# Optimization experiments

Measured on AMD Instinct MI355X. Metric: run time of the kernel, lower is better.

The kernel has to match this reference:

```python
import jax, jax.numpy as jnp
import numpy as np

B, N, D, H = 4, 512, 4, 256


def _linear_params(key, fan_in, fan_out):
    # torch.nn.Linear default init: U(-1/sqrt(fan_in), 1/sqrt(fan_in))
    lim = 1.0 / np.sqrt(fan_in)
    kw, kb = jax.random.split(key)
    W = jax.random.uniform(kw, (fan_in, fan_out), minval=-lim, maxval=lim, dtype=jnp.float32)
    b = jax.random.uniform(kb, (fan_out,), minval=-lim, maxval=lim, dtype=jnp.float32)
    return W, b


def setup_inputs() -> dict:
    key = jax.random.key(0)
    ks = jax.random.split(key, 8)
    x = jax.random.normal(ks[0], (B, N, D), dtype=jnp.float32)
    adj = jax.random.uniform(ks[1], (B, N, N), dtype=jnp.float32)  # soft adjacency in [0,1)
    W_e1, b_e1 = _linear_params(ks[2], 2 * D, H)
    W_e2, b_e2 = _linear_params(ks[3], H, H)
    W_n1, b_n1 = _linear_params(ks[4], H, H)
    W_n2, b_n2 = _linear_params(ks[5], H, H)
    W_o1, b_o1 = _linear_params(ks[6], D + H, H)
    W_o, b_o = _linear_params(ks[7], H, D)
    return {
        "x": x, "adj": adj,
        "W_e1": W_e1, "b_e1": b_e1, "W_e2": W_e2, "b_e2": b_e2,
        "W_n1": W_n1, "b_n1": b_n1, "W_n2": W_n2, "b_n2": b_n2,
        "W_o1": W_o1, "b_o1": b_o1, "W_o": W_o, "b_o": b_o,
    }


def reference(x, adj, W_e1, b_e1, W_e2, b_e2, W_n1, b_n1, W_n2, b_n2, W_o1, b_o1, W_o, b_o):
    b_, n_, d_ = x.shape
    # innode[b,i,j,:] = x[b,j]; outnode[b,i,j,:] = x[b,i]
    innode = jnp.broadcast_to(x[:, None, :, :], (b_, n_, n_, d_))
    outnode = jnp.broadcast_to(x[:, :, None, :], (b_, n_, n_, d_))
    edge_in = jnp.concatenate([innode, outnode], axis=-1)          # [B,N,N,2D]
    node2edge = jax.nn.relu(edge_in @ W_e1 + b_e1)                 # [B,N,N,H]
    edge2edge = jax.nn.relu(node2edge @ W_e2 + b_e2)               # [B,N,N,H]
    # adjacency-masked sum over axis 1 (the i axis)
    agg = jnp.einsum('bij,bijh->bjh', adj, edge2edge)              # [B,N,H]
    out1 = jax.nn.relu(agg @ W_n1 + b_n1)
    out2 = jax.nn.relu(out1 @ W_n2 + b_n2)
    out3 = jnp.concatenate([x, out2], axis=-1)                     # [B,N,D+H]
    out4 = out3 @ W_o1 + b_o1
    out5 = out4 @ W_o + b_o                                        # [B,N,D]
    # CONTINUOUS is False for the classifier variant
    return jax.nn.log_softmax(out5, axis=2)
```

## Files before the change

### kernel.cpp

```cpp
#include <hip/hip_runtime.h>
#include <hip/hip_fp16.h>
#include <math.h>

#define Bq 4
#define Nq 512
#define Dq 4
#define Hq 256

typedef _Float16 f16x8 __attribute__((ext_vector_type(8)));
typedef float f32x4 __attribute__((ext_vector_type(4)));

__device__ __forceinline__ f16x8 hadd_relu(f16x8 u, f16x8 v) {
    f16x8 s = u + v;
    const f16x8 z = (f16x8)(_Float16)0.0f;
    return __builtin_elementwise_max(s, z);
}

__global__ __launch_bounds__(256) void prep_uv(
    const float* __restrict__ x, const float* __restrict__ We1,
    const float* __restrict__ be1, __half* __restrict__ U, __half* __restrict__ V) {
    const int bn = blockIdx.x;
    const int k = threadIdx.x;
    const float* xp = x + bn * Dq;
    const float x0 = xp[0], x1 = xp[1], x2 = xp[2], x3 = xp[3];
    float u = be1[k];
    u = fmaf(x0, We1[0 * 256 + k], u);
    u = fmaf(x1, We1[1 * 256 + k], u);
    u = fmaf(x2, We1[2 * 256 + k], u);
    u = fmaf(x3, We1[3 * 256 + k], u);
    float v = x0 * We1[4 * 256 + k];
    v = fmaf(x1, We1[5 * 256 + k], v);
    v = fmaf(x2, We1[6 * 256 + k], v);
    v = fmaf(x3, We1[7 * 256 + k], v);
    U[(size_t)bn * Hq + k] = __float2half(u);
    V[(size_t)bn * Hq + k] = __float2half(v);
}

__global__ __launch_bounds__(256, 2) void edge_gemm(
    const __half* __restrict__ U, const __half* __restrict__ V,
    const float* __restrict__ We2, const float* __restrict__ be2,
    const float* __restrict__ adj, float* __restrict__ aggws) {
    __shared__ __align__(16) char smem[50176];
    __half* Wt = (__half*)smem;
    __half* Us = (__half*)(smem + 32768);
    __half* Vs = (__half*)(smem + 40960);
    float* adjs = (float*)(smem + 49152);
    float* red = (float*)(smem + 32768);

    const int bid = blockIdx.x;
    const int hq_ = bid & 3;
    const int jt = (bid >> 2) & 31;
    const int b = bid >> 7;
    const int h_base = hq_ * 64;
    const int j_base = jt * 16;
    const int t = threadIdx.x;
    const int lane = t & 63;
    const int w = t >> 6;
    const int q = lane >> 4;
    const int l15 = lane & 15;

    {
        const int n = t & 63;
        const int swz = n & 31;
        for (int kk = (t >> 6); kk < 256; kk += 4) {
            float val = We2[kk * 256 + h_base + n];
            Wt[n * 256 + ((((kk >> 3) ^ swz)) << 3) + (kk & 7)] = __float2half(val);
        }
    }
    {
        const int row = t >> 4;
        const int c0 = (t & 15) * 2;
        const uint4* gp = (const uint4*)(U + (size_t)(b * Nq + j_base + row) * Hq);
        uint4 v0 = gp[c0];
        uint4 v1 = gp[c0 + 1];
        *(uint4*)&Us[row * 256 + ((c0 ^ row) << 3)] = v0;
        *(uint4*)&Us[row * 256 + (((c0 + 1) ^ row) << 3)] = v1;
    }
    __syncthreads();

    f16x8 bfragR[2][8];
#pragma unroll
    for (int nt = 0; nt < 2; ++nt) {
        const int rn = nt * 16 + l15;
#pragma unroll
        for (int ks = 0; ks < 8; ++ks) {
            const int c = ks * 4 + q;
            bfragR[nt][ks] = *(const f16x8*)&Wt[rn * 256 + ((c ^ (rn & 31)) << 3)];
        }
    }

    float bias[4];
#pragma unroll
    for (int nt = 0; nt < 4; ++nt) bias[nt] = be2[h_base + nt * 16 + l15];

    f32x4 agg[4];
#pragma unroll
    for (int nt = 0; nt < 4; ++nt) agg[nt] = (f32x4){0.f, 0.f, 0.f, 0.f};

    const int rn2 = 2 * 16 + l15;
    const int rn3 = 3 * 16 + l15;

    for (int ch = 0; ch < 32; ++ch) {
        const int i_base = ch * 16;
        __syncthreads();
        {
            const int row = t >> 4;
            const int c0 = (t & 15) * 2;
            const uint4* gp = (const uint4*)(V + (size_t)(b * Nq + i_base + row) * Hq);
            uint4 v0 = gp[c0];
            uint4 v1 = gp[c0 + 1];
            *(uint4*)&Vs[row * 256 + ((c0 ^ row) << 3)] = v0;
            *(uint4*)&Vs[row * 256 + (((c0 + 1) ^ row) << 3)] = v1;
        }
        adjs[t] = adj[(size_t)(b * Nq + i_base + (t >> 4)) * Nq + j_base + (t & 15)];
        __syncthreads();

        f32x4 acc[4][4];
#pragma unroll
        for (int mi = 0; mi < 4; ++mi)
#pragma unroll
            for (int nt = 0; nt < 4; ++nt)
                acc[mi][nt] = (f32x4){bias[nt], bias[nt], bias[nt], bias[nt]};

#pragma unroll
        for (int ks = 0; ks < 8; ++ks) {
            const int c = ks * 4 + q;
            const f16x8 uvec = *(const f16x8*)&Us[l15 * 256 + ((c ^ l15) << 3)];
            f16x8 afrag[4];
#pragma unroll
            for (int mi = 0; mi < 4; ++mi) {
                const int iv = w * 4 + mi;
                const f16x8 vvec = *(const f16x8*)&Vs[iv * 256 + ((c ^ iv) << 3)];
                afrag[mi] = hadd_relu(uvec, vvec);
            }
            const f16x8 b2 = *(const f16x8*)&Wt[rn2 * 256 + ((c ^ (rn2 & 31)) << 3)];
            const f16x8 b3 = *(const f16x8*)&Wt[rn3 * 256 + ((c ^ (rn3 & 31)) << 3)];
#pragma unroll
            for (int mi = 0; mi < 4; ++mi) {
                acc[mi][0] = __builtin_amdgcn_mfma_f32_16x16x32_f16(
                    afrag[mi], bfragR[0][ks], acc[mi][0], 0, 0, 0);
                acc[mi][1] = __builtin_amdgcn_mfma_f32_16x16x32_f16(
                    afrag[mi], bfragR[1][ks], acc[mi][1], 0, 0, 0);
                acc[mi][2] = __builtin_amdgcn_mfma_f32_16x16x32_f16(
                    afrag[mi], b2, acc[mi][2], 0, 0, 0);
                acc[mi][3] = __builtin_amdgcn_mfma_f32_16x16x32_f16(
                    afrag[mi], b3, acc[mi][3], 0, 0, 0);
            }
        }

#pragma unroll
        for (int mi = 0; mi < 4; ++mi) {
            const int iv = w * 4 + mi;
            const f32x4 av = *(const f32x4*)&adjs[iv * 16 + q * 4];
#pragma unroll
            for (int nt = 0; nt < 4; ++nt) {
                agg[nt][0] = fmaf(av[0], fmaxf(acc[mi][nt][0], 0.f), agg[nt][0]);
                agg[nt][1] = fmaf(av[1], fmaxf(acc[mi][nt][1], 0.f), agg[nt][1]);
                agg[nt][2] = fmaf(av[2], fmaxf(acc[mi][nt][2], 0.f), agg[nt][2]);
                agg[nt][3] = fmaf(av[3], fmaxf(acc[mi][nt][3], 0.f), agg[nt][3]);
            }
        }
    }

    __syncthreads();
#pragma unroll
    for (int nt = 0; nt < 4; ++nt)
#pragma unroll
        for (int r = 0; r < 4; ++r)
            red[w * 1024 + (q * 4 + r) * 64 + nt * 16 + l15] = agg[nt][r];
    __syncthreads();
    {
        const int j = t >> 4;
        const int h0 = (t & 15) * 4;
        f32x4 s = *(const f32x4*)&red[0 * 1024 + j * 64 + h0];
        s += *(const f32x4*)&red[1 * 1024 + j * 64 + h0];
        s += *(const f32x4*)&red[2 * 1024 + j * 64 + h0];
        s += *(const f32x4*)&red[3 * 1024 + j * 64 + h0];
        *(f32x4*)&aggws[(size_t)(b * Nq + j_base + j) * Hq + h_base + h0] = s;
    }
}

__global__ __launch_bounds__(256) void tail_kernel(
    const float* __restrict__ aggws, const float* __restrict__ x,
    const float* __restrict__ Wn1, const float* __restrict__ bn1,
    const float* __restrict__ Wn2, const float* __restrict__ bn2,
    const float* __restrict__ Wo1, const float* __restrict__ bo1,
    const float* __restrict__ Wo, const float* __restrict__ bo,
    float* __restrict__ out) {
    __shared__ __align__(16) float bufA[256 * 4];
    __shared__ __align__(16) float bufB[256 * 4];
    __shared__ float xs[4][4];
    __shared__ float s5[4][4];
    const int bid = blockIdx.x;
    const int b = bid >> 7;
    const int n0 = (bid & 127) * 4;
    const int t = threadIdx.x;

#pragma unroll
    for (int ni = 0; ni < 4; ++ni)
        bufA[t * 4 + ni] = aggws[(size_t)(b * Nq + n0 + ni) * Hq + t];
    if (t < 16) xs[t >> 2][t & 3] = x[(size_t)(b * Nq + n0 + (t >> 2)) * Dq + (t & 3)];
    __syncthreads();

    float c0, c1, c2, c3;
    c0 = c1 = c2 = c3 = bn1[t];
#pragma unroll 8
    for (int k = 0; k < 256; ++k) {
        const float wv = Wn1[k * 256 + t];
        const float4 av = *(const float4*)&bufA[k * 4];
        c0 = fmaf(av.x, wv, c0); c1 = fmaf(av.y, wv, c1);
        c2 = fmaf(av.z, wv, c2); c3 = fmaf(av.w, wv, c3);
    }
    bufB[t * 4 + 0] = fmaxf(c0, 0.f); bufB[t * 4 + 1] = fmaxf(c1, 0.f);
    bufB[t * 4 + 2] = fmaxf(c2, 0.f); bufB[t * 4 + 3] = fmaxf(c3, 0.f);
    __syncthreads();

    c0 = c1 = c2 = c3 = bn2[t];
#pragma unroll 8
    for (int k = 0; k < 256; ++k) {
        const float wv = Wn2[k * 256 + t];
        const float4 av = *(const float4*)&bufB[k * 4];
        c0 = fmaf(av.x, wv, c0); c1 = fmaf(av.y, wv, c1);
        c2 = fmaf(av.z, wv, c2); c3 = fmaf(av.w, wv, c3);
    }
    bufA[t * 4 + 0] = fmaxf(c0, 0.f); bufA[t * 4 + 1] = fmaxf(c1, 0.f);
    bufA[t * 4 + 2] = fmaxf(c2, 0.f); bufA[t * 4 + 3] = fmaxf(c3, 0.f);
    __syncthreads();

    c0 = c1 = c2 = c3 = bo1[t];
#pragma unroll
    for (int d = 0; d < 4; ++d) {
        const float wv = Wo1[d * 256 + t];
        c0 = fmaf(xs[0][d], wv, c0); c1 = fmaf(xs[1][d], wv, c1);
        c2 = fmaf(xs[2][d], wv, c2); c3 = fmaf(xs[3][d], wv, c3);
    }
#pragma unroll 8
    for (int k = 0; k < 256; ++k) {
        const float wv = Wo1[(4 + k) * 256 + t];
        const float4 av = *(const float4*)&bufA[k * 4];
        c0 = fmaf(av.x, wv, c0); c1 = fmaf(av.y, wv, c1);
        c2 = fmaf(av.z, wv, c2); c3 = fmaf(av.w, wv, c3);
    }
    bufB[t * 4 + 0] = c0; bufB[t * 4 + 1] = c1;
    bufB[t * 4 + 2] = c2; bufB[t * 4 + 3] = c3;
    __syncthreads();

    const int d = t >> 6;
    const int lane = t & 63;
    float p0 = 0.f, p1 = 0.f, p2 = 0.f, p3 = 0.f;
    for (int k = lane; k < 256; k += 64) {
        const float wv = Wo[k * 4 + d];
        const float4 av = *(const float4*)&bufB[k * 4];
        p0 = fmaf(av.x, wv, p0); p1 = fmaf(av.y, wv, p1);
        p2 = fmaf(av.z, wv, p2); p3 = fmaf(av.w, wv, p3);
    }
#pragma unroll
    for (int off = 32; off > 0; off >>= 1) {
        p0 += __shfl_down(p0, off); p1 += __shfl_down(p1, off);
        p2 += __shfl_down(p2, off); p3 += __shfl_down(p3, off);
    }
    if (lane == 0) {
        s5[0][d] = p0 + bo[d]; s5[1][d] = p1 + bo[d];
        s5[2][d] = p2 + bo[d]; s5[3][d] = p3 + bo[d];
    }
    __syncthreads();
    if (t < 4) {
        const float v0 = s5[t][0], v1 = s5[t][1], v2 = s5[t][2], v3 = s5[t][3];
        const float m = fmaxf(fmaxf(v0, v1), fmaxf(v2, v3));
        const float s = expf(v0 - m) + expf(v1 - m) + expf(v2 - m) + expf(v3 - m);
        const float lse = m + logf(s);
        float* op = out + (size_t)(b * Nq + n0 + t) * Dq;
        op[0] = v0 - lse; op[1] = v1 - lse; op[2] = v2 - lse; op[3] = v3 - lse;
    }
}

extern "C" void kernel_launch(void* const* d_in, const int* in_sizes, int n_in,
                              void* d_out, int out_size, void* d_ws, size_t ws_size,
                              hipStream_t stream) {
    const float* x   = (const float*)d_in[0];
    const float* adj = (const float*)d_in[1];
    const float* We1 = (const float*)d_in[2];
    const float* be1 = (const float*)d_in[3];
    const float* We2 = (const float*)d_in[4];
    const float* be2 = (const float*)d_in[5];
    const float* Wn1 = (const float*)d_in[6];
    const float* bn1 = (const float*)d_in[7];
    const float* Wn2 = (const float*)d_in[8];
    const float* bn2 = (const float*)d_in[9];
    const float* Wo1 = (const float*)d_in[10];
    const float* bo1 = (const float*)d_in[11];
    const float* Wo  = (const float*)d_in[12];
    const float* bo  = (const float*)d_in[13];
    float* out = (float*)d_out;

    __half* U = (__half*)d_ws;
    __half* V = U + (size_t)Bq * Nq * Hq;
    float* aggws = (float*)((char*)d_ws + (size_t)2 * Bq * Nq * Hq * sizeof(__half));

    prep_uv<<<Bq * Nq, 256, 0, stream>>>(x, We1, be1, U, V);
    edge_gemm<<<512, 256, 0, stream>>>(U, V, We2, be2, adj, aggws);
    tail_kernel<<<512, 256, 0, stream>>>(aggws, x, Wn1, bn1, Wn2, bn2, Wo1, bo1, Wo, bo, out);
}
```

Baseline: 257.8 us.

## Double-buffer V/adj tiles with register prefetch and keep U fragments in registers

Gives the edge GEMM loop a double-buffered LDS stage for the V rows and adjacency values. The next chunk's global loads are prefetched into registers two iterations ahead and written to the alternate buffer after compute, which drops one barrier per iteration and hides global load latency. The U tile is now loaded straight from global memory into eight register fragments instead of being staged in LDS and re-read every k-step. The cost is higher register pressure (uvec plus the prefetch registers) under launch_bounds(256,2), which could cause spills, and slightly more LDS.

```diff
diff --git a/kernel.cpp b/kernel.cpp
--- a/kernel.cpp
+++ b/kernel.cpp
@@ -40,10 +40,9 @@
     const __half* __restrict__ U, const __half* __restrict__ V,
     const float* __restrict__ We2, const float* __restrict__ be2,
     const float* __restrict__ adj, float* __restrict__ aggws) {
-    __shared__ __align__(16) char smem[50176];
+    __shared__ __align__(16) char smem[51200];
     __half* Wt = (__half*)smem;
-    __half* Us = (__half*)(smem + 32768);
-    __half* Vs = (__half*)(smem + 40960);
+    __half* Vs = (__half*)(smem + 32768);
     float* adjs = (float*)(smem + 49152);
     float* red = (float*)(smem + 32768);
 
@@ -59,6 +58,12 @@
     const int q = lane >> 4;
     const int l15 = lane & 15;
 
+    const __half* Vb = V + (size_t)b * Nq * Hq;
+    const float* adjb = adj + (size_t)b * Nq * Nq;
+
+    const int srow = t >> 4;
+    const int sc0 = (t & 15) * 2;
+
     {
         const int n = t & 63;
         const int swz = n & 31;
@@ -67,15 +72,22 @@
             Wt[n * 256 + ((((kk >> 3) ^ swz)) << 3) + (kk & 7)] = __float2half(val);
         }
     }
-    {
-        const int row = t >> 4;
-        const int c0 = (t & 15) * 2;
-        const uint4* gp = (const uint4*)(U + (size_t)(b * Nq + j_base + row) * Hq);
-        uint4 v0 = gp[c0];
-        uint4 v1 = gp[c0 + 1];
-        *(uint4*)&Us[row * 256 + ((c0 ^ row) << 3)] = v0;
-        *(uint4*)&Us[row * 256 + (((c0 + 1) ^ row) << 3)] = v1;
-    }
+
+    f16x8 uvec[8];
+#pragma unroll
+    for (int ks = 0; ks < 8; ++ks) {
+        const int c = ks * 4 + q;
+        uvec[ks] = *(const f16x8*)&U[(size_t)(b * Nq + j_base + l15) * Hq + c * 8];
+    }
+
+    float bias[4];
+#pragma unroll
+    for (int nt = 0; nt < 4; ++nt) bias[nt] = be2[h_base + nt * 16 + l15];
+
+    f32x4 agg[4];
+#pragma unroll
+    for (int nt = 0; nt < 4; ++nt) agg[nt] = (f32x4){0.f, 0.f, 0.f, 0.f};
+
     __syncthreads();
 
     f16x8 bfragR[2][8];
@@ -88,32 +100,29 @@
             bfragR[nt][ks] = *(const f16x8*)&Wt[rn * 256 + ((c ^ (rn & 31)) << 3)];
         }
     }
-
-    float bias[4];
-#pragma unroll
-    for (int nt = 0; nt < 4; ++nt) bias[nt] = be2[h_base + nt * 16 + l15];
-
-    f32x4 agg[4];
-#pragma unroll
-    for (int nt = 0; nt < 4; ++nt) agg[nt] = (f32x4){0.f, 0.f, 0.f, 0.f};
-
     const int rn2 = 2 * 16 + l15;
     const int rn3 = 3 * 16 + l15;
 
+    uint4 pva, pvb; float pad_;
+    {
+        const uint4* gp = (const uint4*)(Vb + (size_t)(0 + srow) * Hq);
+        pva = gp[sc0]; pvb = gp[sc0 + 1];
+        pad_ = adjb[(size_t)(0 + srow) * Nq + j_base + (t & 15)];
+        *(uint4*)&Vs[0 * 4096 + srow * 256 + ((sc0 ^ srow) << 3)] = pva;
+        *(uint4*)&Vs[0 * 4096 + srow * 256 + (((sc0 + 1) ^ srow) << 3)] = pvb;
+        adjs[0 * 256 + t] = pad_;
+    }
+    {
+        const uint4* gp = (const uint4*)(Vb + (size_t)(16 + srow) * Hq);
+        pva = gp[sc0]; pvb = gp[sc0 + 1];
+        pad_ = adjb[(size_t)(16 + srow) * Nq + j_base + (t & 15)];
+    }
+    __syncthreads();
+
     for (int ch = 0; ch < 32; ++ch) {
-        const int i_base = ch * 16;
-        __syncthreads();
-        {
-            const int row = t >> 4;
-            const int c0 = (t & 15) * 2;
-            const uint4* gp = (const uint4*)(V + (size_t)(b * Nq + i_base + row) * Hq);
-            uint4 v0 = gp[c0];
-            uint4 v1 = gp[c0 + 1];
-            *(uint4*)&Vs[row * 256 + ((c0 ^ row) << 3)] = v0;
-            *(uint4*)&Vs[row * 256 + (((c0 + 1) ^ row) << 3)] = v1;
-        }
-        adjs[t] = adj[(size_t)(b * Nq + i_base + (t >> 4)) * Nq + j_base + (t & 15)];
-        __syncthreads();
+        const int cur = ch & 1;
+        const __half* Vcur = Vs + cur * 4096;
+        const float* Acur = adjs + cur * 256;
 
         f32x4 acc[4][4];
 #pragma unroll
@@ -125,13 +134,12 @@
 #pragma unroll
         for (int ks = 0; ks < 8; ++ks) {
             const int c = ks * 4 + q;
-            const f16x8 uvec = *(const f16x8*)&Us[l15 * 256 + ((c ^ l15) << 3)];
             f16x8 afrag[4];
 #pragma unroll
             for (int mi = 0; mi < 4; ++mi) {
                 const int iv = w * 4 + mi;
-                const f16x8 vvec = *(const f16x8*)&Vs[iv * 256 + ((c ^ iv) << 3)];
-                afrag[mi] = hadd_relu(uvec, vvec);
+                const f16x8 vvec = *(const f16x8*)&Vcur[iv * 256 + ((c ^ iv) << 3)];
+                afrag[mi] = hadd_relu(uvec[ks], vvec);
             }
             const f16x8 b2 = *(const f16x8*)&Wt[rn2 * 256 + ((c ^ (rn2 & 31)) << 3)];
             const f16x8 b3 = *(const f16x8*)&Wt[rn3 * 256 + ((c ^ (rn3 & 31)) << 3)];
@@ -151,7 +159,7 @@
 #pragma unroll
         for (int mi = 0; mi < 4; ++mi) {
             const int iv = w * 4 + mi;
-            const f32x4 av = *(const f32x4*)&adjs[iv * 16 + q * 4];
+            const f32x4 av = *(const f32x4*)&Acur[iv * 16 + q * 4];
 #pragma unroll
             for (int nt = 0; nt < 4; ++nt) {
                 agg[nt][0] = fmaf(av[0], fmaxf(acc[mi][nt][0], 0.f), agg[nt][0]);
@@ -160,9 +168,22 @@
                 agg[nt][3] = fmaf(av[3], fmaxf(acc[mi][nt][3], 0.f), agg[nt][3]);
             }
         }
-    }
-
-    __syncthreads();
+
+        if (ch < 31) {
+            const int nxt = cur ^ 1;
+            *(uint4*)&Vs[nxt * 4096 + srow * 256 + ((sc0 ^ srow) << 3)] = pva;
+            *(uint4*)&Vs[nxt * 4096 + srow * 256 + (((sc0 + 1) ^ srow) << 3)] = pvb;
+            adjs[nxt * 256 + t] = pad_;
+            if (ch < 30) {
+                const int i_base = (ch + 2) * 16;
+                const uint4* gp = (const uint4*)(Vb + (size_t)(i_base + srow) * Hq);
+                pva = gp[sc0]; pvb = gp[sc0 + 1];
+                pad_ = adjb[(size_t)(i_base + srow) * Nq + j_base + (t & 15)];
+            }
+        }
+        __syncthreads();
+    }
+
 #pragma unroll
     for (int nt = 0; nt < 4; ++nt)
 #pragma unroll
```

Measured after the change: 505.1 us. 1.96x slower.
